# Optimization experiments

Measured on AMD Instinct MI355X. Metric: run time of the kernel, lower is better.

## Reference

```python
import jax, jax.numpy as jnp
import numpy as np

B, D_IN = 32, 1024
A, N_PER = 4, 2048
N = A * N_PER
OUT_DIM = 11
THRESHOLD = 0.05
SELF_MASK, CROSS_MASK = 0.8, 0.1


def setup_inputs() -> dict:
    key = jax.random.key(0)
    ks = jax.random.split(key, 8)
    return {
        "x": jax.random.normal(ks[0], (B, D_IN), dtype=jnp.float32),
        "Z0": jax.random.normal(ks[1], (B, A, N_PER), dtype=jnp.float32),
        "receptors_w": jax.random.normal(ks[2], (N, D_IN), dtype=jnp.float32) * 0.02,
        "receptors_b": jax.random.normal(ks[3], (N,), dtype=jnp.float32) * 0.02,
        "synapses_w": jax.random.normal(ks[4], (N, N), dtype=jnp.float32) * 0.02,
        "synapses_b": jax.random.normal(ks[5], (N,), dtype=jnp.float32) * 0.02,
        "output_lobe_w": jax.random.normal(ks[6], (OUT_DIM, N), dtype=jnp.float32) * 0.02,
        "output_lobe_b": jax.random.normal(ks[7], (OUT_DIM,), dtype=jnp.float32) * 0.02,
        "area_idx": jnp.arange(N, dtype=jnp.int64).reshape(A, N_PER),
    }


def reference(x, Z0, receptors_w, receptors_b, synapses_w, synapses_b,
              output_lobe_w, output_lobe_b, area_idx):
    # area_idx: [A, n] partition of neurons into areas; perm: [N]
    perm = area_idx.reshape(-1)
    b = x.shape[0]

    # stimulus[i] = F.linear(x, receptors_w[idx_i], receptors_b[idx_i]),
    # computed for all areas at once then reshaped to per-area blocks.
    stim_flat = x @ receptors_w.T + receptors_b          # [B, N]
    stim = stim_flat[:, perm].reshape(b, A, N_PER)        # [B, A, n]

    # threshold gate per source area: |Z|.mean() > threshold (predicated)
    gate = (jnp.mean(jnp.abs(Z0), axis=(0, 2)) > THRESHOLD).astype(Z0.dtype)  # [A]

    # per-(out,in)-block synapse weights with clamped mask scale
    Wp = synapses_w[perm][:, perm].reshape(A, N_PER, A, N_PER)  # [A,n,A,n]
    scale = jnp.where(jnp.eye(A, dtype=bool), SELF_MASK, CROSS_MASK)  # [A,A]
    Weff = Wp * scale[:, None, :, None]

    # Z_next[out] = sum_in gate[in] * (Z[in] @ Weff[out,:,in,:].T) + gate[out]*bias[out]
    Zg = Z0 * gate[None, :, None]                         # [B, A, n]
    Znext = jnp.einsum('onam,bam->bon', Weff, Zg)         # [B, A, n]
    bias_blocks = synapses_b[perm].reshape(A, N_PER)      # diagonal-block bias
    Znext = Znext + gate[:, None] * bias_blocks           # fires with in==out gate

    Znew = jnp.tanh(Znext + stim)                         # [B, A, n]

    # scatter per-area state back into flat neuron order
    Z_flat = jnp.zeros((b, N), dtype=Znew.dtype).at[:, perm].set(Znew.reshape(b, N))

    raw = Z_flat @ output_lobe_w.T + output_lobe_b        # [B, 11]
    logits = raw[:, :10]
    out_gate = jax.nn.sigmoid(raw[:, 10])
    return logits, out_gate
```

## Files before the change

kernel.cpp:

```cpp
#include <hip/hip_runtime.h>
#include <math.h>

#define BATCH 32
#define DIN   1024
#define NPER  2048
#define NTOT  8192
#define KTOT  9216
#define NCHUNK 288

typedef __attribute__((ext_vector_type(8))) short short8;
typedef __attribute__((ext_vector_type(4))) float f32x4;

__device__ __forceinline__ unsigned short f2bf(float f) {
  unsigned u = __float_as_uint(f);
  u += 0x7FFF + ((u >> 16) & 1);
  return (unsigned short)(u >> 16);
}

__global__ void k_gate(const float* __restrict__ Z0, float* __restrict__ gsum) {
  const int a = blockIdx.x >> 3;
  const int slice = blockIdx.x & 7;
  const int tid = threadIdx.x;
  float s = 0.f;
#pragma unroll
  for (int it = 0; it < 8; ++it) {
    const int idx = it * 256 + tid;
    const int b = slice * 4 + (idx >> 9);
    const int n4 = idx & 511;
    const float4 z = *(const float4*)(Z0 + (size_t)b * NTOT + a * NPER + n4 * 4);
    s += fabsf(z.x) + fabsf(z.y) + fabsf(z.z) + fabsf(z.w);
  }
#pragma unroll
  for (int off = 32; off > 0; off >>= 1) s += __shfl_down(s, off);
  __shared__ float wsum[4];
  if ((tid & 63) == 0) wsum[tid >> 6] = s;
  __syncthreads();
  if (tid == 0) atomicAdd(&gsum[a], wsum[0] + wsum[1] + wsum[2] + wsum[3]);
}

__global__ void k_prep(const float* __restrict__ Z0, const float* __restrict__ x,
                       const float* __restrict__ gsum, unsigned short* __restrict__ zg) {
  const int idx = blockIdx.x * 256 + threadIdx.x;
  const int b = idx / (KTOT / 4);
  const int k = (idx % (KTOT / 4)) * 4;
  float4 v; float g;
  if (k < NTOT) {
    v = *(const float4*)(Z0 + (size_t)b * NTOT + k);
    g = (gsum[k >> 11] * (1.f / (BATCH * NPER)) > 0.05f) ? 1.f : 0.f;
  } else {
    v = *(const float4*)(x + (size_t)b * DIN + (k - NTOT));
    g = 1.f;
  }
  ushort4 o;
  o.x = f2bf(v.x * g); o.y = f2bf(v.y * g);
  o.z = f2bf(v.z * g); o.w = f2bf(v.w * g);
  *(ushort4*)(zg + (size_t)b * KTOT + k) = o;
}

__launch_bounds__(512, 4)
__global__ void k_main(const float* __restrict__ Rw, const float* __restrict__ rbias,
                       const float* __restrict__ Sw, const float* __restrict__ sbias,
                       const float* __restrict__ gsum, const unsigned short* __restrict__ zg,
                       float* __restrict__ Zn) {
  const int tid = threadIdx.x;
  const int w = tid >> 6, lane = tid & 63;
  const int m = lane & 15, quad = lane >> 4;
  const int r0 = blockIdx.x * 16;
  const int o = r0 >> 11;

  float g[4];
#pragma unroll
  for (int a = 0; a < 4; ++a)
    g[a] = (gsum[a] * (1.f / (BATCH * NPER)) > 0.05f) ? 1.f : 0.f;
  const float c0 = g[0] * ((o == 0) ? 0.8f : 0.1f);
  const float c1 = g[1] * ((o == 1) ? 0.8f : 0.1f);
  const float c2 = g[2] * ((o == 2) ? 0.8f : 0.1f);
  const float c3 = g[3] * ((o == 3) ? 0.8f : 0.1f);

  const float* swrow = Sw + (size_t)(r0 + m) * NTOT;
  const float* rwrow = Rw + (size_t)(r0 + m) * DIN;
  const unsigned short* zg0 = zg + (size_t)m * KTOT;
  const unsigned short* zg1 = zg + (size_t)(m + 16) * KTOT;

  f32x4 acc0 = {0.f, 0.f, 0.f, 0.f};
  f32x4 acc1 = {0.f, 0.f, 0.f, 0.f};

  for (int c = w; c < NCHUNK; c += 8) {
    const int k0 = c * 32;
    const float* ap; float s;
    if (k0 < NTOT) {
      ap = swrow + k0;
      const int a = k0 >> 11;
      s = (a == 0) ? c0 : (a == 1) ? c1 : (a == 2) ? c2 : c3;
    } else {
      ap = rwrow + (k0 - NTOT);
      s = 1.f;
    }
    const float4 wv0 = *(const float4*)(ap + quad * 8);
    const float4 wv1 = *(const float4*)(ap + quad * 8 + 4);
    short8 af;
    af[0] = (short)f2bf(wv0.x * s); af[1] = (short)f2bf(wv0.y * s);
    af[2] = (short)f2bf(wv0.z * s); af[3] = (short)f2bf(wv0.w * s);
    af[4] = (short)f2bf(wv1.x * s); af[5] = (short)f2bf(wv1.y * s);
    af[6] = (short)f2bf(wv1.z * s); af[7] = (short)f2bf(wv1.w * s);
    const short8 bf0 = *(const short8*)(zg0 + k0 + quad * 8);
    const short8 bf1 = *(const short8*)(zg1 + k0 + quad * 8);
    acc0 = __builtin_amdgcn_mfma_f32_16x16x32_bf16(af, bf0, acc0, 0, 0, 0);
    acc1 = __builtin_amdgcn_mfma_f32_16x16x32_bf16(af, bf1, acc1, 0, 0, 0);
  }

  __shared__ float red[8][2][16][16];
#pragma unroll
  for (int r = 0; r < 4; ++r) {
    red[w][0][quad * 4 + r][m] = acc0[r];
    red[w][1][quad * 4 + r][m] = acc1[r];
  }
  __syncthreads();
  const int mrow = tid >> 5, n = tid & 31;
  const int f = n >> 4, nn = n & 15;
  float v = 0.f;
#pragma unroll
  for (int ww = 0; ww < 8; ++ww) v += red[ww][f][mrow][nn];
  const int r = r0 + mrow;
  const float gate_o = (o == 0) ? g[0] : (o == 1) ? g[1] : (o == 2) ? g[2] : g[3];
  v += rbias[r] + gate_o * sbias[r];
  Zn[(size_t)r * BATCH + n] = tanhf(v);
}

__global__ void k_proj(const float* __restrict__ Zn, const float* __restrict__ olw,
                       float* __restrict__ raw) {
  const int j = blockIdx.x >> 4;
  const int rs = blockIdx.x & 15;
  const int tid = threadIdx.x;
  const int b = tid & 31, stripe = tid >> 5;
  const int rbase = rs * 512 + stripe * 64;
  float a = 0.f;
#pragma unroll
  for (int rr = 0; rr < 64; ++rr) {
    const int r = rbase + rr;
    a = fmaf(olw[j * NTOT + r], Zn[(size_t)r * BATCH + b], a);
  }
  __shared__ float red[8][33];
  red[stripe][b] = a;
  __syncthreads();
  if (stripe == 0) {
    float v = 0.f;
#pragma unroll
    for (int s2 = 0; s2 < 8; ++s2) v += red[s2][b];
    atomicAdd(&raw[j * BATCH + b], v);
  }
}

__global__ void k_fin(const float* __restrict__ raw, const float* __restrict__ olb,
                      float* __restrict__ out) {
  const int t = threadIdx.x;
  if (t < 352) {
    const int j = t >> 5, b = t & 31;
    const float v = raw[j * BATCH + b] + olb[j];
    if (j < 10) out[b * 10 + j] = v;
    else        out[320 + b] = 1.f / (1.f + expf(-v));
  }
}

extern "C" void kernel_launch(void* const* d_in, const int* in_sizes, int n_in,
                              void* d_out, int out_size, void* d_ws, size_t ws_size,
                              hipStream_t stream) {
  const float* x    = (const float*)d_in[0];
  const float* Z0   = (const float*)d_in[1];
  const float* Rw   = (const float*)d_in[2];
  const float* rb_  = (const float*)d_in[3];
  const float* Sw   = (const float*)d_in[4];
  const float* sb_  = (const float*)d_in[5];
  const float* olw  = (const float*)d_in[6];
  const float* olb  = (const float*)d_in[7];

  float* ws   = (float*)d_ws;
  float* gsum = ws;
  float* raw  = ws + 8;
  float* Zn   = ws + 512;
  unsigned short* zg = (unsigned short*)(ws + 512 + NTOT * BATCH);

  hipMemsetAsync(d_ws, 0, 512 * sizeof(float), stream);
  k_gate<<<32, 256, 0, stream>>>(Z0, gsum);
  k_prep<<<BATCH * KTOT / 1024, 256, 0, stream>>>(Z0, x, gsum, zg);
  k_main<<<NTOT / 16, 512, 0, stream>>>(Rw, rb_, Sw, sb_, gsum, zg, Zn);
  k_proj<<<11 * 16, 256, 0, stream>>>(Zn, olw, raw);
  k_fin<<<1, 384, 0, stream>>>(raw, olb, (float*)d_out);
}
```

Baseline: 421.2 us.

## Stage weight tiles into LDS via async global_load_lds with double buffering

The main GEMM kernel now streams each 16-row by 256-column fp32 weight tile into shared memory with direct global-to-LDS loads, double-buffered so the next chunk loads while the current one is converted and fed to MFMA. Block size drops from 512 to 256 threads and the cross-wave reduction is reorganized to fit. The goal is fully coalesced, asynchronous streaming of the large synapse matrix, which bounds this kernel's memory traffic. The cost is a barrier per chunk and LDS usage that may limit occupancy, while the activation operand still comes straight from global memory.

```diff
diff --git a/kernel.cpp b/kernel.cpp
--- a/kernel.cpp
+++ b/kernel.cpp
@@ -6,10 +6,19 @@
 #define NPER  2048
 #define NTOT  8192
 #define KTOT  9216
-#define NCHUNK 288
+#define KC    256
+#define NCH   36
+#define AROW  260
 
 typedef __attribute__((ext_vector_type(8))) short short8;
 typedef __attribute__((ext_vector_type(4))) float f32x4;
+
+typedef __attribute__((address_space(1))) const unsigned int gu32_t;
+typedef __attribute__((address_space(3))) unsigned int su32_t;
+
+__device__ __forceinline__ void load_lds16(const float* g, float* l) {
+  __builtin_amdgcn_global_load_lds((gu32_t*)g, (su32_t*)l, 16, 0, 0);
+}
 
 __device__ __forceinline__ unsigned short f2bf(float f) {
   unsigned u = __float_as_uint(f);
@@ -57,74 +66,86 @@
   *(ushort4*)(zg + (size_t)b * KTOT + k) = o;
 }
 
-__launch_bounds__(512, 4)
+__launch_bounds__(256, 4)
 __global__ void k_main(const float* __restrict__ Rw, const float* __restrict__ rbias,
                        const float* __restrict__ Sw, const float* __restrict__ sbias,
                        const float* __restrict__ gsum, const unsigned short* __restrict__ zg,
                        float* __restrict__ Zn) {
+  __shared__ __align__(16) float As[2][16][AROW];
+  __shared__ float red[8][16][17];
   const int tid = threadIdx.x;
   const int w = tid >> 6, lane = tid & 63;
   const int m = lane & 15, quad = lane >> 4;
   const int r0 = blockIdx.x * 16;
   const int o = r0 >> 11;
 
-  float g[4];
-#pragma unroll
-  for (int a = 0; a < 4; ++a)
+  float g[4], coeff[4];
+#pragma unroll
+  for (int a = 0; a < 4; ++a) {
     g[a] = (gsum[a] * (1.f / (BATCH * NPER)) > 0.05f) ? 1.f : 0.f;
-  const float c0 = g[0] * ((o == 0) ? 0.8f : 0.1f);
-  const float c1 = g[1] * ((o == 1) ? 0.8f : 0.1f);
-  const float c2 = g[2] * ((o == 2) ? 0.8f : 0.1f);
-  const float c3 = g[3] * ((o == 3) ? 0.8f : 0.1f);
-
-  const float* swrow = Sw + (size_t)(r0 + m) * NTOT;
-  const float* rwrow = Rw + (size_t)(r0 + m) * DIN;
+    coeff[a] = g[a] * ((a == o) ? 0.8f : 0.1f);
+  }
+
+  auto stage = [&](int c, int buf) {
+    const int k0 = c * KC;
+    const float* base; int rs;
+    if (k0 < NTOT) { base = Sw + (size_t)r0 * NTOT + k0;          rs = NTOT; }
+    else           { base = Rw + (size_t)r0 * DIN + (k0 - NTOT);  rs = DIN;  }
+#pragma unroll
+    for (int i = 0; i < 4; ++i) {
+      const int r = w * 4 + i;
+      load_lds16(base + (size_t)r * rs + lane * 4, &As[buf][r][0]);
+    }
+  };
+
+  f32x4 acc0 = {0.f, 0.f, 0.f, 0.f};
+  f32x4 acc1 = {0.f, 0.f, 0.f, 0.f};
+
   const unsigned short* zg0 = zg + (size_t)m * KTOT;
   const unsigned short* zg1 = zg + (size_t)(m + 16) * KTOT;
 
-  f32x4 acc0 = {0.f, 0.f, 0.f, 0.f};
-  f32x4 acc1 = {0.f, 0.f, 0.f, 0.f};
-
-  for (int c = w; c < NCHUNK; c += 8) {
-    const int k0 = c * 32;
-    const float* ap; float s;
-    if (k0 < NTOT) {
-      ap = swrow + k0;
-      const int a = k0 >> 11;
-      s = (a == 0) ? c0 : (a == 1) ? c1 : (a == 2) ? c2 : c3;
-    } else {
-      ap = rwrow + (k0 - NTOT);
-      s = 1.f;
+  stage(0, 0);
+  for (int c = 0; c < NCH; ++c) {
+    const int buf = c & 1;
+    __syncthreads();
+    if (c + 1 < NCH) stage(c + 1, buf ^ 1);
+    const float s = (c < 32) ? coeff[c >> 3] : 1.f;
+#pragma unroll
+    for (int u = 0; u < 2; ++u) {
+      const int ks = (w * 2 + u) * 32;
+      const float* ap = &As[buf][m][ks + quad * 8];
+      const float4 a0 = *(const float4*)ap;
+      const float4 a1 = *(const float4*)(ap + 4);
+      short8 af;
+      af[0] = (short)f2bf(a0.x * s); af[1] = (short)f2bf(a0.y * s);
+      af[2] = (short)f2bf(a0.z * s); af[3] = (short)f2bf(a0.w * s);
+      af[4] = (short)f2bf(a1.x * s); af[5] = (short)f2bf(a1.y * s);
+      af[6] = (short)f2bf(a1.z * s); af[7] = (short)f2bf(a1.w * s);
+      const int kg = c * KC + ks + quad * 8;
+      const short8 b0 = *(const short8*)(zg0 + kg);
+      const short8 b1 = *(const short8*)(zg1 + kg);
+      acc0 = __builtin_amdgcn_mfma_f32_16x16x32_bf16(af, b0, acc0, 0, 0, 0);
+      acc1 = __builtin_amdgcn_mfma_f32_16x16x32_bf16(af, b1, acc1, 0, 0, 0);
     }
-    const float4 wv0 = *(const float4*)(ap + quad * 8);
-    const float4 wv1 = *(const float4*)(ap + quad * 8 + 4);
-    short8 af;
-    af[0] = (short)f2bf(wv0.x * s); af[1] = (short)f2bf(wv0.y * s);
-    af[2] = (short)f2bf(wv0.z * s); af[3] = (short)f2bf(wv0.w * s);
-    af[4] = (short)f2bf(wv1.x * s); af[5] = (short)f2bf(wv1.y * s);
-    af[6] = (short)f2bf(wv1.z * s); af[7] = (short)f2bf(wv1.w * s);
-    const short8 bf0 = *(const short8*)(zg0 + k0 + quad * 8);
-    const short8 bf1 = *(const short8*)(zg1 + k0 + quad * 8);
-    acc0 = __builtin_amdgcn_mfma_f32_16x16x32_bf16(af, bf0, acc0, 0, 0, 0);
-    acc1 = __builtin_amdgcn_mfma_f32_16x16x32_bf16(af, bf1, acc1, 0, 0, 0);
-  }
-
-  __shared__ float red[8][2][16][16];
+  }
+
 #pragma unroll
   for (int r = 0; r < 4; ++r) {
-    red[w][0][quad * 4 + r][m] = acc0[r];
-    red[w][1][quad * 4 + r][m] = acc1[r];
+    red[w * 2 + 0][quad * 4 + r][m] = acc0[r];
+    red[w * 2 + 1][quad * 4 + r][m] = acc1[r];
   }
   __syncthreads();
-  const int mrow = tid >> 5, n = tid & 31;
-  const int f = n >> 4, nn = n & 15;
-  float v = 0.f;
-#pragma unroll
-  for (int ww = 0; ww < 8; ++ww) v += red[ww][f][mrow][nn];
-  const int r = r0 + mrow;
-  const float gate_o = (o == 0) ? g[0] : (o == 1) ? g[1] : (o == 2) ? g[2] : g[3];
-  v += rbias[r] + gate_o * sbias[r];
-  Zn[(size_t)r * BATCH + n] = tanhf(v);
+  const float gate_o = g[o];
+#pragma unroll
+  for (int t = tid; t < 512; t += 256) {
+    const int row = t >> 5, n = t & 31;
+    const int h = n >> 4, nn = n & 15;
+    float v = red[0 + h][row][nn] + red[2 + h][row][nn] +
+              red[4 + h][row][nn] + red[6 + h][row][nn];
+    const int r = r0 + row;
+    v += rbias[r] + gate_o * sbias[r];
+    Zn[(size_t)r * BATCH + n] = tanhf(v);
+  }
 }
 
 __global__ void k_proj(const float* __restrict__ Zn, const float* __restrict__ olw,
@@ -183,7 +204,7 @@
   hipMemsetAsync(d_ws, 0, 512 * sizeof(float), stream);
   k_gate<<<32, 256, 0, stream>>>(Z0, gsum);
   k_prep<<<BATCH * KTOT / 1024, 256, 0, stream>>>(Z0, x, gsum, zg);
-  k_main<<<NTOT / 16, 512, 0, stream>>>(Rw, rb_, Sw, sb_, gsum, zg, Zn);
+  k_main<<<NTOT / 16, 256, 0, stream>>>(Rw, rb_, Sw, sb_, gsum, zg, Zn);
   k_proj<<<11 * 16, 256, 0, stream>>>(Zn, olw, raw);
   k_fin<<<1, 384, 0, stream>>>(raw, olb, (float*)d_out);
 }
```

After: 410.6 us. 2.5% less time.
